# Kernel tuning notes

Hardware: AMD Instinct MI355X
Metric: run time of the kernel (lower is better)

Reference implementation:

```python
import jax, jax.numpy as jnp
import numpy as np

N_SRC, N_DST, E = 50000, 50000, 800000
D_GT, D_AG = 64, 64
HID, HEADS = 256, 4
FPH = HID // HEADS  # 64
N_ACT = 16
NEG_SLOPE = 0.2  # DGL GATv2Conv default negative_slope


def setup_inputs() -> dict:
    key = jax.random.key(0)
    ks = jax.random.split(key, 16)
    f32 = jnp.float32
    return {
        "feat_gt": jax.random.normal(ks[0], (N_SRC, D_GT), f32),
        "feat_agent": jax.random.normal(ks[1], (N_DST, D_AG), f32),
        "h0": jax.random.normal(ks[2], (N_DST, HID), f32),
        "edge_src": jax.random.randint(ks[3], (E,), 0, N_SRC),
        "edge_dst": jax.random.randint(ks[4], (E,), 0, N_DST),
        "W_src": jax.random.normal(ks[5], (D_GT, HID), f32) * 0.1,
        "b_src": jnp.zeros((HID,), f32),
        "W_dst": jax.random.normal(ks[6], (D_AG, HID), f32) * 0.1,
        "b_dst": jnp.zeros((HID,), f32),
        "attn": jax.random.normal(ks[7], (HEADS, FPH), f32) * 0.1,
        "W_res": jax.random.normal(ks[8], (D_AG, HID), f32) * 0.1,
        "b_res": jnp.zeros((HID,), f32),
        "W_ih": jax.random.normal(ks[9], (3 * HID, HID), f32) * 0.05,
        "W_hh": jax.random.normal(ks[10], (3 * HID, HID), f32) * 0.05,
        "b_ih": jnp.zeros((3 * HID,), f32),
        "b_hh": jnp.zeros((3 * HID,), f32),
        "W_out": jax.random.normal(ks[11], (HID, N_ACT), f32) * 0.05,
        "b_out": jnp.zeros((N_ACT,), f32),
    }


def _gatv2(feat_gt, feat_agent, edge_src, edge_dst,
           W_src, b_src, W_dst, b_dst, attn, W_res, b_res):
    # GATv2Conv (bipartite, share_weights=False, residual=True, activation=ReLU)
    fs = (feat_gt @ W_src + b_src).reshape(N_SRC, HEADS, FPH)    # [Ns,H,F]
    fd = (feat_agent @ W_dst + b_dst).reshape(N_DST, HEADS, FPH)  # [Nd,H,F]
    e = fs[edge_src] + fd[edge_dst]                               # [E,H,F]
    e = jnp.where(e > 0, e, NEG_SLOPE * e)                        # LeakyReLU
    score = jnp.einsum('ehf,hf->eh', e, attn)                     # [E,H]
    # edge softmax segmented by destination node
    smax = jax.lax.stop_gradient(
        jax.ops.segment_max(score, edge_dst, num_segments=N_DST))  # [Nd,H]
    ex = jnp.exp(score - smax[edge_dst])
    den = jax.ops.segment_sum(ex, edge_dst, num_segments=N_DST)   # [Nd,H]
    alpha = ex / den[edge_dst]                                    # [E,H]
    msg = alpha[:, :, None] * fs[edge_src]                        # [E,H,F]
    rst = jax.ops.segment_sum(msg, edge_dst, num_segments=N_DST)  # [Nd,H,F]
    rst = rst.reshape(N_DST, HID) + (feat_agent @ W_res + b_res)  # residual
    return jax.nn.relu(rst)


def _gru_cell(x, h, W_ih, W_hh, b_ih, b_hh):
    gi = x @ W_ih.T + b_ih
    gh = h @ W_hh.T + b_hh
    ir, iz, inn = jnp.split(gi, 3, axis=-1)
    hr, hz, hn = jnp.split(gh, 3, axis=-1)
    r = jax.nn.sigmoid(ir + hr)
    z = jax.nn.sigmoid(iz + hz)
    n = jnp.tanh(inn + r * hn)
    return (1.0 - z) * n + z * h


def reference(feat_gt, feat_agent, h0, edge_src, edge_dst,
              W_src, b_src, W_dst, b_dst, attn, W_res, b_res,
              W_ih, W_hh, b_ih, b_hh, W_out, b_out):
    x = _gatv2(feat_gt, feat_agent, edge_src, edge_dst,
               W_src, b_src, W_dst, b_dst, attn, W_res, b_res)  # [Nd,HID]
    h = _gru_cell(x, h0, W_ih, W_hh, b_ih, b_hh)                # [Nd,HID]
    logits = h @ W_out + b_out                                  # [Nd,N_ACT]
    return (logits, h)
```

## Files before the change

### kernel.cpp

```cpp
#include <hip/hip_runtime.h>
#include <stdint.h>

#define N_SRCN 50000
#define N_DSTN 50000
#define NE     800000
#define HIDN   256
#define NEG    0.2f

typedef __attribute__((ext_vector_type(8)))  short short8;
typedef __attribute__((ext_vector_type(16))) float float16v;

__device__ __forceinline__ float bf2f(unsigned short u){
    union { unsigned u32; float f; } c; c.u32 = ((unsigned)u) << 16; return c.f;
}
__device__ __forceinline__ unsigned short f2bf(float f){
    union { float f; unsigned u; } c; c.f = f;
    unsigned r = c.u + 0x7fffu + ((c.u >> 16) & 1u);
    return (unsigned short)(r >> 16);
}
__device__ __forceinline__ float4 ld4b(const unsigned short* p){
    uint2 u = *reinterpret_cast<const uint2*>(p);
    float4 r;
    r.x = bf2f((unsigned short)(u.x & 0xffff));
    r.y = bf2f((unsigned short)(u.x >> 16));
    r.z = bf2f((unsigned short)(u.y & 0xffff));
    r.w = bf2f((unsigned short)(u.y >> 16));
    return r;
}
__device__ __forceinline__ void unpack8(uint4 u, float* f){
    f[0] = bf2f((unsigned short)(u.x & 0xffff)); f[1] = bf2f((unsigned short)(u.x >> 16));
    f[2] = bf2f((unsigned short)(u.y & 0xffff)); f[3] = bf2f((unsigned short)(u.y >> 16));
    f[4] = bf2f((unsigned short)(u.z & 0xffff)); f[5] = bf2f((unsigned short)(u.z >> 16));
    f[6] = bf2f((unsigned short)(u.w & 0xffff)); f[7] = bf2f((unsigned short)(u.w >> 16));
}
__device__ __forceinline__ void gload_lds16(const unsigned short* g, unsigned short* l){
    __builtin_amdgcn_global_load_lds(
        (const __attribute__((address_space(1))) void*)g,
        (__attribute__((address_space(3))) void*)l,
        16, 0, 0);
}

__global__ void pack_kernel(const float* __restrict__ Wsrc, const float* __restrict__ Wdst,
                            const float* __restrict__ Wres, const float* __restrict__ Wih,
                            const float* __restrict__ Whh,
                            unsigned short* __restrict__ Wt2,
                            unsigned short* __restrict__ Wf){
    int i = blockIdx.x * 256 + threadIdx.x;
    if (i < 49152){
        int which = i >> 14, j = i & 16383;
        int k = j >> 8, c = j & 255;
        const float* W = (which == 0) ? Wsrc : (which == 1 ? Wdst : Wres);
        float v = W[j];
        int off = which * 16384 + (c >> 5) * 2048 + (k >> 4) * 512
                + (((k >> 3) & 1) * 32 + (c & 31)) * 8 + (k & 7);
        Wt2[off] = f2bf(v);
    } else if (i < 49152 + 196608){
        int o = i - 49152;
        int row = o >> 8, k = o & 255;
        int g = row >> 8, c = row & 255;
        float v = Wih[o];
        int off = (c >> 5) * 49152 + (k >> 4) * 1536 + g * 512
                + (((k >> 3) & 1) * 32 + (c & 31)) * 8 + (k & 7);
        Wf[off] = f2bf(v);
    } else if (i < 49152 + 393216){
        int o = i - 49152 - 196608;
        int row = o >> 8, k = o & 255;
        int g = row >> 8, c = row & 255;
        float v = Whh[o];
        int off = (c >> 5) * 49152 + (16 + (k >> 4)) * 1536 + g * 512
                + (((k >> 3) & 1) * 32 + (c & 31)) * 8 + (k & 7);
        Wf[off] = f2bf(v);
    }
}

__global__ __launch_bounds__(256) void proj_kernel(
        const float* __restrict__ Agt, const float* __restrict__ Aag,
        const unsigned short* __restrict__ Wt2,
        const float* __restrict__ bsrc, const float* __restrict__ bdst,
        const float* __restrict__ bres,
        unsigned short* __restrict__ fs, unsigned short* __restrict__ fd,
        unsigned short* __restrict__ resb){
    __shared__ unsigned short As[64 * 72];
    __shared__ unsigned short Cs[64 * 72];
    int z = blockIdx.z;
    const float* A = (z == 0) ? Agt : Aag;
    const float* bias = (z == 0) ? bsrc : (z == 1 ? bdst : bres);
    unsigned short* out = (z == 0) ? fs : (z == 1 ? fd : resb);
    const unsigned short* Wb = Wt2 + z * 16384;
    int tid = threadIdx.x;
    int m0 = blockIdx.y * 64;
    #pragma unroll
    for (int i = 0; i < 4; ++i){
        int ci = tid + i * 256;
        int row = ci >> 4;
        int k4 = (ci & 15) << 2;
        int gr = m0 + row; if (gr >= N_SRCN) gr = N_SRCN - 1;
        float4 v = *reinterpret_cast<const float4*>(A + (size_t)gr * 64 + k4);
        unsigned short* dp = As + row * 72 + k4;
        dp[0] = f2bf(v.x); dp[1] = f2bf(v.y); dp[2] = f2bf(v.z); dp[3] = f2bf(v.w);
    }
    __syncthreads();
    int lane = tid & 63, w = tid >> 6;
    int l31 = lane & 31, half = lane >> 5;
    int msub = (w & 1) * 32;
    int cbw = blockIdx.x * 2 + (w >> 1);
    const unsigned short* bb = Wb + cbw * 2048 + lane * 8;
    const unsigned short* ap = As + (msub + l31) * 72 + half * 8;
    float16v acc = {0,0,0,0,0,0,0,0,0,0,0,0,0,0,0,0};
    #pragma unroll
    for (int ks = 0; ks < 4; ++ks){
        short8 a = *reinterpret_cast<const short8*>(ap + ks * 16);
        short8 b = *reinterpret_cast<const short8*>(bb + ks * 512);
        acc = __builtin_amdgcn_mfma_f32_32x32x16_bf16(a, b, acc, 0, 0, 0);
    }
    float bv = bias[cbw * 32 + l31];
    int ccol = (w >> 1) * 32 + l31;
    #pragma unroll
    for (int r = 0; r < 16; ++r){
        int row = (r & 3) + 8 * (r >> 2) + 4 * half + msub;
        Cs[row * 72 + ccol] = f2bf(acc[r] + bv);
    }
    __syncthreads();
    int srow = tid >> 2, chunk = tid & 3;
    int gr2 = m0 + srow;
    if (gr2 < N_SRCN){
        const uint4* sp = reinterpret_cast<const uint4*>(Cs + srow * 72 + chunk * 16);
        uint4* gp = reinterpret_cast<uint4*>(out + (size_t)gr2 * 256 + blockIdx.x * 64 + chunk * 16);
        gp[0] = sp[0];
        gp[1] = sp[1];
    }
}

__global__ void degree_kernel(const int* __restrict__ dst, int* __restrict__ deg){
    int i = blockIdx.x * 256 + threadIdx.x;
    if (i < NE) atomicAdd(&deg[dst[i]], 1);
}

__global__ void scan1_kernel(const int* __restrict__ deg, int* __restrict__ bsum){
    __shared__ int s[256];
    int tid = threadIdx.x;
    int i = blockIdx.x * 256 + tid;
    s[tid] = (i < N_DSTN) ? deg[i] : 0;
    __syncthreads();
    #pragma unroll
    for (int off = 128; off; off >>= 1){
        if (tid < off) s[tid] += s[tid + off];
        __syncthreads();
    }
    if (tid == 0) bsum[blockIdx.x] = s[0];
}

__global__ void scan2_kernel(const int* __restrict__ bsum, int* __restrict__ boff){
    __shared__ int s[256];
    int tid = threadIdx.x;
    int v = (tid < 196) ? bsum[tid] : 0;
    s[tid] = v;
    __syncthreads();
    #pragma unroll
    for (int off = 1; off < 256; off <<= 1){
        int t = (tid >= off) ? s[tid - off] : 0;
        __syncthreads();
        s[tid] += t;
        __syncthreads();
    }
    if (tid < 196) boff[tid] = s[tid] - v;
}

__global__ void scan3_kernel(const int* __restrict__ deg, const int* __restrict__ boff,
                             int* __restrict__ ptr, int* __restrict__ cursor){
    __shared__ int s[256];
    int tid = threadIdx.x;
    int i = blockIdx.x * 256 + tid;
    int v = (i < N_DSTN) ? deg[i] : 0;
    s[tid] = v;
    __syncthreads();
    #pragma unroll
    for (int off = 1; off < 256; off <<= 1){
        int t = (tid >= off) ? s[tid - off] : 0;
        __syncthreads();
        s[tid] += t;
        __syncthreads();
    }
    int ex = s[tid] - v + boff[blockIdx.x];
    if (i < N_DSTN){ ptr[i] = ex; cursor[i] = ex; }
}

__global__ void scatter_kernel(const int* __restrict__ src, const int* __restrict__ dst,
                               int* __restrict__ cursor, int* __restrict__ csr){
    int i = blockIdx.x * 256 + threadIdx.x;
    if (i < NE){
        int d = dst[i];
        int pos = atomicAdd(&cursor[d], 1);
        csr[pos] = src[i];
    }
}

__global__ __launch_bounds__(256) void aggregate_kernel(
        const unsigned short* __restrict__ fs, const unsigned short* __restrict__ fd,
        const unsigned short* __restrict__ res, const float* __restrict__ attn,
        const int* __restrict__ ptr, const int* __restrict__ deg,
        const int* __restrict__ csr, unsigned short* __restrict__ x){
    int wv = threadIdx.x >> 6;
    int d = blockIdx.x * 4 + wv;
    if (d >= N_DSTN) return;
    int lane = threadIdx.x & 63;
    int s = lane >> 5;
    int sl = lane & 31;
    int c8 = sl * 8;
    float fdv[8];
    unpack8(*reinterpret_cast<const uint4*>(fd + (size_t)d * 256 + c8), fdv);
    const float* atp = attn + (sl >> 3) * 64 + (sl & 7) * 8;
    float4 at0 = *reinterpret_cast<const float4*>(atp);
    float4 at1 = *reinterpret_cast<const float4*>(atp + 4);
    float at[8] = {at0.x, at0.y, at0.z, at0.w, at1.x, at1.y, at1.z, at1.w};
    int p = ptr[d], dg = deg[d];
    float lsum = 0.f;
    float acc[8] = {0.f, 0.f, 0.f, 0.f, 0.f, 0.f, 0.f, 0.f};
    for (int base = 0; base < dg; base += 64){
        int cnt = min(64, dg - base);
        int sreg = (lane < cnt) ? csr[p + base + lane] : 0;
        uint4 cur = *reinterpret_cast<const uint4*>(
            fs + (size_t)__shfl(sreg, s) * 256 + c8);
        for (int j = 0; j < cnt; j += 2){
            uint4 nxt = *reinterpret_cast<const uint4*>(
                fs + (size_t)__shfl(sreg, (j + 2 + s) & 63) * 256 + c8);
            float b[8];
            unpack8(cur, b);
            float part = 0.f;
            #pragma unroll
            for (int i = 0; i < 8; ++i){
                float e = b[i] + fdv[i];
                e = (e > 0.f) ? e : NEG * e;
                part = fmaf(e, at[i], part);
            }
            part += __shfl_xor(part, 1);
            part += __shfl_xor(part, 2);
            part += __shfl_xor(part, 4);
            float wgt = ((j + s) < cnt) ? __expf(part) : 0.f;
            lsum += wgt;
            #pragma unroll
            for (int i = 0; i < 8; ++i) acc[i] = fmaf(wgt, b[i], acc[i]);
            cur = nxt;
        }
    }
    lsum += __shfl_xor(lsum, 32);
    #pragma unroll
    for (int i = 0; i < 8; ++i) acc[i] += __shfl_xor(acc[i], 32);
    float inv = (lsum > 0.f) ? 1.f / lsum : 0.f;
    float rv[8];
    unpack8(*reinterpret_cast<const uint4*>(res + (size_t)d * 256 + c8), rv);
    unsigned short ob[8];
    #pragma unroll
    for (int i = 0; i < 8; ++i)
        ob[i] = f2bf(fmaxf(fmaf(acc[i], inv, rv[i]), 0.f));
    if (s == 0){
        uint4 o;
        o.x = (unsigned)ob[0] | ((unsigned)ob[1] << 16);
        o.y = (unsigned)ob[2] | ((unsigned)ob[3] << 16);
        o.z = (unsigned)ob[4] | ((unsigned)ob[5] << 16);
        o.w = (unsigned)ob[6] | ((unsigned)ob[7] << 16);
        *reinterpret_cast<uint4*>(x + (size_t)d * 256 + c8) = o;
    }
}

__global__ __launch_bounds__(512, 4) void gru_kernel(
        const unsigned short* __restrict__ Xb,
        const float* __restrict__ H0, const unsigned short* __restrict__ Wf,
        const float* __restrict__ bih, const float* __restrict__ bhh,
        float* __restrict__ outH){
    __shared__ unsigned short As[2 * 32 * 256];
    int tid = threadIdx.x;
    int m0 = blockIdx.x << 5;
    int w = tid >> 6, lane = tid & 63;

    #pragma unroll
    for (int i = 0; i < 2; ++i){
        int g = w + i * 8;
        int row = 2 * g + (lane >> 5);
        int gr = m0 + row; if (gr >= N_DSTN) gr = N_DSTN - 1;
        int j = lane & 31;
        const unsigned short* src = Xb + (size_t)gr * 256 + ((j ^ (row & 15)) << 3);
        gload_lds16(src, As + g * 512);
    }
    {
        int hrow = tid >> 4, hseg = tid & 15;
        int hgr = m0 + hrow; if (hgr >= N_DSTN) hgr = N_DSTN - 1;
        const float* hp = H0 + (size_t)hgr * 256 + hseg * 16;
        float4 f0 = *reinterpret_cast<const float4*>(hp);
        float4 f1 = *reinterpret_cast<const float4*>(hp + 4);
        float4 f2 = *reinterpret_cast<const float4*>(hp + 8);
        float4 f3 = *reinterpret_cast<const float4*>(hp + 12);
        int rl = hrow & 15;
        int c0 = hseg * 2;
        uint4 o;
        o.x = (unsigned)f2bf(f0.x) | ((unsigned)f2bf(f0.y) << 16);
        o.y = (unsigned)f2bf(f0.z) | ((unsigned)f2bf(f0.w) << 16);
        o.z = (unsigned)f2bf(f1.x) | ((unsigned)f2bf(f1.y) << 16);
        o.w = (unsigned)f2bf(f1.z) | ((unsigned)f2bf(f1.w) << 16);
        *reinterpret_cast<uint4*>(As + 8192 + hrow * 256 + ((c0 ^ rl) << 3)) = o;
        o.x = (unsigned)f2bf(f2.x) | ((unsigned)f2bf(f2.y) << 16);
        o.y = (unsigned)f2bf(f2.z) | ((unsigned)f2bf(f2.w) << 16);
        o.z = (unsigned)f2bf(f3.x) | ((unsigned)f2bf(f3.y) << 16);
        o.w = (unsigned)f2bf(f3.z) | ((unsigned)f2bf(f3.w) << 16);
        *reinterpret_cast<uint4*>(As + 8192 + hrow * 256 + (((c0 + 1) ^ rl) << 3)) = o;
    }
    asm volatile("s_waitcnt vmcnt(0) lgkmcnt(0)" ::: "memory");
    __syncthreads();

    int l31 = lane & 31, half = lane >> 5;
    int ct = w;
    int rl = l31 & 15;
    const unsigned short* bb = Wf + ct * 49152 + lane * 8;
    float16v zv = {0,0,0,0,0,0,0,0,0,0,0,0,0,0,0,0};
    float16v ar = zv, az = zv, anx = zv, anh = zv;
    #pragma unroll
    for (int p = 0; p < 32; ++p){
        const unsigned short* bp = bb + p * 1536;
        short8 vr = *reinterpret_cast<const short8*>(bp);
        short8 vz = *reinterpret_cast<const short8*>(bp + 512);
        short8 vn = *reinterpret_cast<const short8*>(bp + 1024);
        const unsigned short* ap_ = (p < 16) ? As : (As + 8192);
        int kl = p & 15;
        short8 a = *reinterpret_cast<const short8*>(
                       ap_ + l31 * 256 + (((kl * 2 + half) ^ rl) << 3));
        ar = __builtin_amdgcn_mfma_f32_32x32x16_bf16(a, vr, ar, 0, 0, 0);
        az = __builtin_amdgcn_mfma_f32_32x32x16_bf16(a, vz, az, 0, 0, 0);
        if (p < 16) anx = __builtin_amdgcn_mfma_f32_32x32x16_bf16(a, vn, anx, 0, 0, 0);
        else        anh = __builtin_amdgcn_mfma_f32_32x32x16_bf16(a, vn, anh, 0, 0, 0);
    }
    int cg = ct * 32 + l31;
    float rb = bih[cg] + bhh[cg];
    float zb = bih[256 + cg] + bhh[256 + cg];
    float bin = bih[512 + cg], bhn = bhh[512 + cg];
    #pragma unroll
    for (int r = 0; r < 16; ++r){
        int m = m0 + (r & 3) + 8 * (r >> 2) + 4 * half;
        if (m < N_DSTN){
            float h0v = H0[(size_t)m * 256 + cg];
            float rrg = 1.f / (1.f + __expf(-(ar[r] + rb)));
            float zg  = 1.f / (1.f + __expf(-(az[r] + zb)));
            float nx = anx[r] + bin + rrg * (anh[r] + bhn);
            float tm = __expf(-2.f * fabsf(nx));
            float nn = (1.f - tm) / (1.f + tm);
            nn = (nx >= 0.f) ? nn : -nn;
            outH[(size_t)m * 256 + cg] = (1.f - zg) * nn + zg * h0v;
        }
    }
}

__global__ __launch_bounds__(256) void logits_kernel(
        const float* __restrict__ H, const float* __restrict__ Wout,
        const float* __restrict__ bout, float* __restrict__ outL){
    __shared__ float Hl[16 * 260];
    __shared__ float Wl[16 * 260];
    int tid = threadIdx.x;
    int m0 = blockIdx.x * 16;
    #pragma unroll
    for (int i = 0; i < 4; ++i){
        int ci = tid + i * 256;
        int row = ci >> 6;
        int c4 = (ci & 63) << 2;
        int gr = m0 + row; if (gr >= N_DSTN) gr = N_DSTN - 1;
        float4 v = *reinterpret_cast<const float4*>(H + (size_t)gr * 256 + c4);
        float* dp = Hl + row * 260 + c4;
        dp[0] = v.x; dp[1] = v.y; dp[2] = v.z; dp[3] = v.w;
    }
    #pragma unroll
    for (int i = 0; i < 16; ++i){
        int ci = tid + i * 256;
        int c = ci >> 4, j = ci & 15;
        Wl[j * 260 + c] = Wout[c * 16 + j];
    }
    __syncthreads();
    int row = tid >> 4, j = tid & 15;
    const float* hr = Hl + row * 260;
    const float* wr = Wl + j * 260;
    float acc = bout[j];
    #pragma unroll
    for (int c = 0; c < 256; c += 4){
        float4 hv = *reinterpret_cast<const float4*>(hr + c);
        float4 wv = *reinterpret_cast<const float4*>(wr + c);
        acc = fmaf(hv.x, wv.x, fmaf(hv.y, wv.y, fmaf(hv.z, wv.z, fmaf(hv.w, wv.w, acc))));
    }
    int m = m0 + row;
    if (m < N_DSTN) outL[m * 16 + j] = acc;
}

extern "C" void kernel_launch(void* const* d_in, const int* in_sizes, int n_in,
                              void* d_out, int out_size, void* d_ws, size_t ws_size,
                              hipStream_t stream){
    const float* feat_gt = (const float*)d_in[0];
    const float* feat_ag = (const float*)d_in[1];
    const float* h0      = (const float*)d_in[2];
    const int*   e_src   = (const int*)d_in[3];
    const int*   e_dst   = (const int*)d_in[4];
    const float* W_src   = (const float*)d_in[5];
    const float* b_src   = (const float*)d_in[6];
    const float* W_dst   = (const float*)d_in[7];
    const float* b_dst   = (const float*)d_in[8];
    const float* attn    = (const float*)d_in[9];
    const float* W_res   = (const float*)d_in[10];
    const float* b_res   = (const float*)d_in[11];
    const float* W_ih    = (const float*)d_in[12];
    const float* W_hh    = (const float*)d_in[13];
    const float* b_ih    = (const float*)d_in[14];
    const float* b_hh    = (const float*)d_in[15];
    const float* W_out   = (const float*)d_in[16];
    const float* b_out   = (const float*)d_in[17];

    float* outL = (float*)d_out;
    float* outH = outL + (size_t)N_DSTN * 16;

    char* ws = (char*)d_ws;
    size_t off = 0;
    auto alloc = [&](size_t bytes) -> void* {
        void* p = ws + off; off = (off + bytes + 255) & ~(size_t)255; return p;
    };
    unsigned short* fs   = (unsigned short*)alloc((size_t)N_SRCN * 256 * 2);
    unsigned short* fd   = (unsigned short*)alloc((size_t)N_DSTN * 256 * 2);
    unsigned short* res  = (unsigned short*)alloc((size_t)N_DSTN * 256 * 2);
    unsigned short* xb   = (unsigned short*)alloc((size_t)N_DSTN * 256 * 2);
    unsigned short* Wt2  = (unsigned short*)alloc(49152 * 2);
    unsigned short* Wf   = (unsigned short*)alloc(393216 * 2);
    int* deg    = (int*)alloc(N_DSTN * 4);
    int* ptr    = (int*)alloc(N_DSTN * 4);
    int* cursor = (int*)alloc(N_DSTN * 4);
    int* csr    = (int*)alloc((size_t)NE * 4);
    int* bsum   = (int*)alloc(256 * 4);
    int* boff   = (int*)alloc(256 * 4);

    hipMemsetAsync(deg, 0, N_DSTN * 4, stream);
    pack_kernel<<<1728, 256, 0, stream>>>(W_src, W_dst, W_res, W_ih, W_hh, Wt2, Wf);

    proj_kernel<<<dim3(4, 782, 3), 256, 0, stream>>>(feat_gt, feat_ag, Wt2,
                                                     b_src, b_dst, b_res, fs, fd, res);

    degree_kernel<<<3125, 256, 0, stream>>>(e_dst, deg);
    scan1_kernel<<<196, 256, 0, stream>>>(deg, bsum);
    scan2_kernel<<<1, 256, 0, stream>>>(bsum, boff);
    scan3_kernel<<<196, 256, 0, stream>>>(deg, boff, ptr, cursor);
    scatter_kernel<<<3125, 256, 0, stream>>>(e_src, e_dst, cursor, csr);
    aggregate_kernel<<<12500, 256, 0, stream>>>(fs, fd, res, attn, ptr, deg, csr, xb);

    gru_kernel<<<1563, 512, 0, stream>>>(xb, h0, Wf, b_ih, b_hh, outH);
    logits_kernel<<<3125, 256, 0, stream>>>(outH, W_out, b_out, outL);
}
```

Baseline: 445.8 us.

## Deepen gather prefetch in aggregation and loop column tiles inside projection blocks

The aggregate kernel now prefetches four neighbour rows per half-wave (eight edges in flight per wave) rather than one, and uses 512-thread blocks covering eight destinations. This is meant to hide gather latency on the random fs reads. The projection kernel loops over all four 64-column tiles inside each block, so the A tile is converted and staged to LDS once per row block instead of four times. The extra rows read past the degree count are masked out of the weights but still fetched, and the wider blocks and deeper prefetch raise register pressure.

```diff
diff --git a/kernel.cpp b/kernel.cpp
--- a/kernel.cpp
+++ b/kernel.cpp
@@ -82,13 +82,13 @@
         unsigned short* __restrict__ resb){
     __shared__ unsigned short As[64 * 72];
     __shared__ unsigned short Cs[64 * 72];
-    int z = blockIdx.z;
+    int z = blockIdx.y;
     const float* A = (z == 0) ? Agt : Aag;
     const float* bias = (z == 0) ? bsrc : (z == 1 ? bdst : bres);
     unsigned short* out = (z == 0) ? fs : (z == 1 ? fd : resb);
     const unsigned short* Wb = Wt2 + z * 16384;
     int tid = threadIdx.x;
-    int m0 = blockIdx.y * 64;
+    int m0 = blockIdx.x * 64;
     #pragma unroll
     for (int i = 0; i < 4; ++i){
         int ci = tid + i * 256;
@@ -103,31 +103,34 @@
     int lane = tid & 63, w = tid >> 6;
     int l31 = lane & 31, half = lane >> 5;
     int msub = (w & 1) * 32;
-    int cbw = blockIdx.x * 2 + (w >> 1);
-    const unsigned short* bb = Wb + cbw * 2048 + lane * 8;
     const unsigned short* ap = As + (msub + l31) * 72 + half * 8;
-    float16v acc = {0,0,0,0,0,0,0,0,0,0,0,0,0,0,0,0};
-    #pragma unroll
-    for (int ks = 0; ks < 4; ++ks){
-        short8 a = *reinterpret_cast<const short8*>(ap + ks * 16);
-        short8 b = *reinterpret_cast<const short8*>(bb + ks * 512);
-        acc = __builtin_amdgcn_mfma_f32_32x32x16_bf16(a, b, acc, 0, 0, 0);
-    }
-    float bv = bias[cbw * 32 + l31];
-    int ccol = (w >> 1) * 32 + l31;
-    #pragma unroll
-    for (int r = 0; r < 16; ++r){
-        int row = (r & 3) + 8 * (r >> 2) + 4 * half + msub;
-        Cs[row * 72 + ccol] = f2bf(acc[r] + bv);
-    }
-    __syncthreads();
     int srow = tid >> 2, chunk = tid & 3;
     int gr2 = m0 + srow;
-    if (gr2 < N_SRCN){
-        const uint4* sp = reinterpret_cast<const uint4*>(Cs + srow * 72 + chunk * 16);
-        uint4* gp = reinterpret_cast<uint4*>(out + (size_t)gr2 * 256 + blockIdx.x * 64 + chunk * 16);
-        gp[0] = sp[0];
-        gp[1] = sp[1];
+    for (int xb = 0; xb < 4; ++xb){
+        if (xb) __syncthreads();
+        int cbw = xb * 2 + (w >> 1);
+        const unsigned short* bb = Wb + cbw * 2048 + lane * 8;
+        float16v acc = {0,0,0,0,0,0,0,0,0,0,0,0,0,0,0,0};
+        #pragma unroll
+        for (int ks = 0; ks < 4; ++ks){
+            short8 a = *reinterpret_cast<const short8*>(ap + ks * 16);
+            short8 b = *reinterpret_cast<const short8*>(bb + ks * 512);
+            acc = __builtin_amdgcn_mfma_f32_32x32x16_bf16(a, b, acc, 0, 0, 0);
+        }
+        float bv = bias[cbw * 32 + l31];
+        int ccol = (w >> 1) * 32 + l31;
+        #pragma unroll
+        for (int r = 0; r < 16; ++r){
+            int row = (r & 3) + 8 * (r >> 2) + 4 * half + msub;
+            Cs[row * 72 + ccol] = f2bf(acc[r] + bv);
+        }
+        __syncthreads();
+        if (gr2 < N_SRCN){
+            const uint4* sp = reinterpret_cast<const uint4*>(Cs + srow * 72 + chunk * 16);
+            uint4* gp = reinterpret_cast<uint4*>(out + (size_t)gr2 * 256 + xb * 64 + chunk * 16);
+            gp[0] = sp[0];
+            gp[1] = sp[1];
+        }
     }
 }
 
@@ -195,13 +198,13 @@
     }
 }
 
-__global__ __launch_bounds__(256) void aggregate_kernel(
+__global__ __launch_bounds__(512) void aggregate_kernel(
         const unsigned short* __restrict__ fs, const unsigned short* __restrict__ fd,
         const unsigned short* __restrict__ res, const float* __restrict__ attn,
         const int* __restrict__ ptr, const int* __restrict__ deg,
         const int* __restrict__ csr, unsigned short* __restrict__ x){
     int wv = threadIdx.x >> 6;
-    int d = blockIdx.x * 4 + wv;
+    int d = blockIdx.x * 8 + wv;
     if (d >= N_DSTN) return;
     int lane = threadIdx.x & 63;
     int s = lane >> 5;
@@ -219,29 +222,39 @@
     for (int base = 0; base < dg; base += 64){
         int cnt = min(64, dg - base);
         int sreg = (lane < cnt) ? csr[p + base + lane] : 0;
-        uint4 cur = *reinterpret_cast<const uint4*>(
-            fs + (size_t)__shfl(sreg, s) * 256 + c8);
-        for (int j = 0; j < cnt; j += 2){
-            uint4 nxt = *reinterpret_cast<const uint4*>(
-                fs + (size_t)__shfl(sreg, (j + 2 + s) & 63) * 256 + c8);
-            float b[8];
-            unpack8(cur, b);
-            float part = 0.f;
-            #pragma unroll
-            for (int i = 0; i < 8; ++i){
-                float e = b[i] + fdv[i];
-                e = (e > 0.f) ? e : NEG * e;
-                part = fmaf(e, at[i], part);
-            }
-            part += __shfl_xor(part, 1);
-            part += __shfl_xor(part, 2);
-            part += __shfl_xor(part, 4);
-            float wgt = ((j + s) < cnt) ? __expf(part) : 0.f;
-            lsum += wgt;
-            #pragma unroll
-            for (int i = 0; i < 8; ++i) acc[i] = fmaf(wgt, b[i], acc[i]);
-            cur = nxt;
+#define GROW(IDX) (*reinterpret_cast<const uint4*>( \
+            fs + (size_t)__shfl(sreg, (IDX) & 63) * 256 + c8))
+        uint4 b0 = GROW(0 + s);
+        uint4 b1 = GROW(2 + s);
+        uint4 b2 = GROW(4 + s);
+        uint4 b3 = GROW(6 + s);
+        for (int j = 0; j < cnt; j += 8){
+            uint4 n0 = GROW(j + 8 + s);
+            uint4 n1 = GROW(j + 10 + s);
+            uint4 n2 = GROW(j + 12 + s);
+            uint4 n3 = GROW(j + 14 + s);
+#define PROC(BV, IDX) { \
+            float b[8]; unpack8(BV, b); \
+            float part = 0.f; \
+            _Pragma("unroll") \
+            for (int i = 0; i < 8; ++i){ \
+                float e = b[i] + fdv[i]; \
+                e = (e > 0.f) ? e : NEG * e; \
+                part = fmaf(e, at[i], part); \
+            } \
+            part += __shfl_xor(part, 1); \
+            part += __shfl_xor(part, 2); \
+            part += __shfl_xor(part, 4); \
+            float wgt = ((IDX) < cnt) ? __expf(part) : 0.f; \
+            lsum += wgt; \
+            _Pragma("unroll") \
+            for (int i = 0; i < 8; ++i) acc[i] = fmaf(wgt, b[i], acc[i]); }
+            PROC(b0, j + 0 + s) PROC(b1, j + 2 + s)
+            PROC(b2, j + 4 + s) PROC(b3, j + 6 + s)
+#undef PROC
+            b0 = n0; b1 = n1; b2 = n2; b3 = n3;
         }
+#undef GROW
     }
     lsum += __shfl_xor(lsum, 32);
     #pragma unroll
@@ -432,15 +445,15 @@
     hipMemsetAsync(deg, 0, N_DSTN * 4, stream);
     pack_kernel<<<1728, 256, 0, stream>>>(W_src, W_dst, W_res, W_ih, W_hh, Wt2, Wf);
 
-    proj_kernel<<<dim3(4, 782, 3), 256, 0, stream>>>(feat_gt, feat_ag, Wt2,
-                                                     b_src, b_dst, b_res, fs, fd, res);
+    proj_kernel<<<dim3(782, 3), 256, 0, stream>>>(feat_gt, feat_ag, Wt2,
+                                                  b_src, b_dst, b_res, fs, fd, res);
 
     degree_kernel<<<3125, 256, 0, stream>>>(e_dst, deg);
     scan1_kernel<<<196, 256, 0, stream>>>(deg, bsum);
     scan2_kernel<<<1, 256, 0, stream>>>(bsum, boff);
     scan3_kernel<<<196, 256, 0, stream>>>(deg, boff, ptr, cursor);
     scatter_kernel<<<3125, 256, 0, stream>>>(e_src, e_dst, cursor, csr);
-    aggregate_kernel<<<12500, 256, 0, stream>>>(fs, fd, res, attn, ptr, deg, csr, xb);
+    aggregate_kernel<<<6250, 512, 0, stream>>>(fs, fd, res, attn, ptr, deg, csr, xb);
 
     gru_kernel<<<1563, 512, 0, stream>>>(xb, h0, Wf, b_ih, b_hh, outH);
     logits_kernel<<<3125, 256, 0, stream>>>(outH, W_out, b_out, outL);
```

Result: no change. 445.5 us (-0.1%).
